# Kernel optimization log

Hardware: AMD Instinct MI355X
Metric: run time of the kernel (lower is better)

## Reference

```python
import jax, jax.numpy as jnp
import numpy as np

T, B, V, S = 800, 32, 1024, 100
BLANK = 0
LS = 0.1
NEG = -1e10  # finite 'log-zero' to keep grads NaN-free


def setup_inputs() -> dict:
    key = jax.random.key(0)
    k1, k2, k3, k4 = jax.random.split(key, 4)
    logits = jax.random.normal(k1, (T, B, V), jnp.float32)
    log_probs = jax.nn.log_softmax(logits, axis=-1)  # (T,B,V) as F.ctc_loss expects
    targets = jax.random.randint(k2, (B, S), 1, V)   # non-blank labels
    input_lengths = jax.random.randint(k3, (B,), T // 2, T + 1)
    target_lengths = jax.random.randint(k4, (B,), S // 2, S + 1)
    return dict(log_probs=log_probs, targets=targets,
                input_lengths=input_lengths, target_lengths=target_lengths)


def _ctc_loss_mean(log_probs, targets, input_lengths, target_lengths):
    # log_probs: (T,B,V); targets: (B,S)
    Tt, Bb, Vv = log_probs.shape
    Ss = targets.shape[1]
    L = 2 * Ss + 1  # extended label sequence: blank-interleaved
    ext = jnp.full((Bb, L), BLANK, dtype=targets.dtype).at[:, 1::2].set(targets)
    ext_prev2 = jnp.pad(ext[:, :-2], ((0, 0), (2, 0)), constant_values=BLANK)
    # transition s-2 -> s allowed only for non-blank labels differing from two back
    can_skip = (ext != BLANK) & (ext != ext_prev2)  # (B,L)

    def emit(lp_t):  # (B,V) -> (B,L) emission log-probs of extended labels
        return jnp.take_along_axis(lp_t, ext, axis=1)

    e0 = emit(log_probs[0])
    alpha0 = jnp.full((Bb, L), NEG, dtype=log_probs.dtype)
    alpha0 = alpha0.at[:, 0].set(e0[:, 0]).at[:, 1].set(e0[:, 1])

    def step(alpha, xs):
        lp_t, t = xs
        a1 = jnp.pad(alpha[:, :-1], ((0, 0), (1, 0)), constant_values=NEG)
        a2 = jnp.pad(alpha[:, :-2], ((0, 0), (2, 0)), constant_values=NEG)
        new = jnp.logaddexp(alpha, a1)
        new = jnp.where(can_skip, jnp.logaddexp(new, a2), new) + emit(lp_t)
        # freeze alpha for t >= input_length so final carry == alpha at len-1
        alpha = jnp.where((t < input_lengths)[:, None], new, alpha)
        return alpha, None

    alpha_T, _ = jax.lax.scan(step, alpha0, (log_probs[1:], jnp.arange(1, Tt)))

    idx = 2 * target_lengths  # final blank position in extended sequence
    a_blank = jnp.take_along_axis(alpha_T, idx[:, None], axis=1)[:, 0]
    a_label = jnp.take_along_axis(alpha_T, (idx - 1)[:, None], axis=1)[:, 0]
    nll = -jnp.logaddexp(a_blank, a_label)  # (B,)
    nll = jnp.where(nll > 1e9, 0.0, nll)    # zero_infinity
    # reduction='mean': per-sample loss / target_length, then batch mean
    return jnp.mean(nll / target_lengths.astype(log_probs.dtype))


def reference(log_probs, targets, input_lengths, target_lengths):
    ctc = _ctc_loss_mean(log_probs, targets, input_lengths, target_lengths)
    smooth = -jnp.mean(log_probs)
    return (1.0 - LS) * ctc + LS * smooth
```

## Files before the change

kernel.cpp:

```cpp
#include <hip/hip_runtime.h>
#include <hip/hip_bf16.h>

#define T_DIM 800
#define B_DIM 32
#define V_DIM 1024
#define S_DIM 100
#define L2E  1.4426950408889634f
#define LN2  0.6931471805599453f

#define NB1  1600
#define EOFF 4096
#define EROW 128
#define BROWS 801


__device__ __forceinline__ float dpp_shr1_f(float x) {
    return __int_as_float(__builtin_amdgcn_update_dpp(
        0, __float_as_int(x), 0x138, 0xF, 0xF, false));
}
__device__ __forceinline__ int dpp_shr1_i(int x) {
    return __builtin_amdgcn_update_dpp(0, x, 0x138, 0xF, 0xF, false);
}
__device__ __forceinline__ float rl50(float x) {
    return __int_as_float(__builtin_amdgcn_readlane(__float_as_int(x), 50));
}
__device__ __forceinline__ void gl16(const float* g, float* lds_dst) {
    __builtin_amdgcn_global_load_lds(
        (const __attribute__((address_space(1))) unsigned int*)g,
        (__attribute__((address_space(3))) unsigned int*)lds_dst,
        16, 0, 0);
}

extern "C" __global__ void __launch_bounds__(256)
ctc_prep(const float* __restrict__ lp,
         const int* __restrict__ tgt,
         float* __restrict__ ws)
{
    __shared__ float rb[4][V_DIM];
    __shared__ float red[4];
    float* E = ws + EOFF;
    float* partials = ws + 1;
    const int bid = blockIdx.x;
    const int tid = threadIdx.x;
    const int w = tid >> 6, j = tid & 63;
    const int b  = bid / 50;
    const int t0 = (bid - b * 50) * 16 + w * 4;
    const int* tg = tgt + b * S_DIM;

    if (bid == 0 && tid == 0) ((unsigned int*)ws)[0] = 0;

    int c1 = 0, c2 = 0;
    if (j <= 49) { int2 t2 = ((const int2*)tg)[j]; c1 = t2.x; c2 = t2.y; }

    const float* base = lp + ((size_t)t0 * B_DIM + b) * V_DIM;
    const size_t RSTRIDE = (size_t)B_DIM * V_DIM;

    const float4* s0 = (const float4*)base;
    float4 A = s0[j], Bv = s0[j + 64], C = s0[j + 128], D = s0[j + 192];

    float s = 0.0f;
    #pragma unroll
    for (int i = 0; i < 4; ++i) {
        float4 A2 = A, B2 = Bv, C2 = C, D2 = D;
        if (i < 3) {
            const float4* sn = (const float4*)(base + (size_t)(i + 1) * RSTRIDE);
            A2 = sn[j]; B2 = sn[j + 64]; C2 = sn[j + 128]; D2 = sn[j + 192];
        }
        s += ((A.x + A.y) + (A.z + A.w)) + ((Bv.x + Bv.y) + (Bv.z + Bv.w))
           + ((C.x + C.y) + (C.z + C.w)) + ((D.x + D.y) + (D.z + D.w));
        float* rw = rb[w];
        ((float4*)rw)[j] = A; ((float4*)rw)[j + 64] = Bv;
        ((float4*)rw)[j + 128] = C; ((float4*)rw)[j + 192] = D;
        float a, c;
        if (j <= 49)      { a = __builtin_amdgcn_exp2f(rw[c1] * L2E);
                            c = __builtin_amdgcn_exp2f(rw[c2] * L2E); }
        else if (j == 50) { float ebv = __builtin_amdgcn_exp2f(rw[0] * L2E);
                            a = ebv; c = ebv; }
        else              { a = 0.0f; c = 0.0f; }
        ((float2*)(E + ((size_t)b * BROWS + t0 + i) * EROW))[j] = make_float2(a, c);
        A = A2; Bv = B2; C = C2; D = D2;
    }
    for (int off = 32; off; off >>= 1) s += __shfl_down(s, off, 64);
    if (j == 0) red[w] = s;
    __syncthreads();
    if (tid == 0) partials[bid] = (red[0] + red[1]) + (red[2] + red[3]);
}

extern "C" __global__ void __launch_bounds__(128)
ctc_rec(const int* __restrict__ tgt,
        const int* __restrict__ ilen,
        const int* __restrict__ tlen,
        float* __restrict__ ws,
        float* __restrict__ out)
{
    __shared__ float bufA[32 * EROW];
    __shared__ float bufB[32 * EROW];
    unsigned int* cnt = (unsigned int*)ws;
    float* partials = ws + 1;
    float* nlls = ws + 1 + NB1;
    const int b = blockIdx.x;
    const int tid = threadIdx.x;
    const int wav = tid >> 6;
    const int l = tid & 63;
    const float* E = ws + EOFF + (size_t)b * BROWS * EROW;
    const int* tg = tgt + b * S_DIM;
    const int len = ilen[b];
    const int tl  = tlen[b];
    const int steps = len - 1;
    const int nfull = steps >> 5;
    const int nst   = steps & 31;
    const int N     = nfull + (nst ? 1 : 0);

#define STAGE_P(BUFP, SB) do { \
    const int tb_ = 1 + 32 * (SB); \
    float* bp_ = (BUFP); \
    _Pragma("unroll") \
    for (int g_ = 0; g_ < 16; ++g_) { \
        gl16(E + (size_t)(tb_ + 2 * g_) * EROW + 4 * l, bp_ + g_ * 256); \
    } \
} while (0)

#define WAIT0 do { \
    asm volatile("s_waitcnt vmcnt(0)" ::: "memory"); \
    __builtin_amdgcn_sched_barrier(0); \
} while (0)

    if (wav == 1) {
        STAGE_P(bufA, 0); WAIT0;
        __builtin_amdgcn_s_barrier();
        #pragma unroll 1
        for (int k = 1; k < N; ++k) {
            STAGE_P((k & 1) ? bufB : bufA, k); WAIT0;
            __builtin_amdgcn_s_barrier();
        }
        return;
    }

    float cs1f = 0, cs3f = 0;
    if (l <= 49) {
        int v1 = tg[2 * l];
        int vp = (l >= 1) ? tg[2 * l - 1] : -1;
        cs1f = (v1 != vp) ? 1.0f : 0.0f;
        int v3 = tg[2 * l + 1];
        cs3f = (v3 != v1) ? 1.0f : 0.0f;
    }

    float p0 = 0, p1 = 0, p2 = 0, p3 = 0;
    float qv = 0, sff = 0, sfg = 0;
    int   el = 0, eLp = 0;
    {
        float2 q0 = ((const float2*)E)[l];
        float eb0 = rl50(q0.x);
        p0 = (l == 0) ? eb0  : 0.0f;
        p1 = (l == 0) ? q0.x : 0.0f;
    }

    float2 ga0, ga1, ga2, ga3, gb0, gb1, gb2, gb3;

#define PREF_(BUF, G, R0, R1, R2, R3) do { \
    const float2* bp_ = (const float2*)(BUF); \
    R0 = bp_[(4 * (G) + 0) * 64 + l]; \
    R1 = bp_[(4 * (G) + 1) * 64 + l]; \
    R2 = bp_[(4 * (G) + 2) * 64 + l]; \
    R3 = bp_[(4 * (G) + 3) * 64 + l]; \
} while (0)

#define BD do { \
    float mz_ = fmaxf(fmaxf(p0, p1), fmaxf(p2, p3)); \
    int dead_ = (mz_ == 0.0f) ? 1 : 0; \
    int er_ = (int)((__float_as_uint(mz_) >> 23) & 255u); \
    unsigned fld_ = dead_ ? 127u : (unsigned)(254 - er_); \
    float sc_ = __uint_as_float(fld_ << 23); \
    p0 *= sc_; p1 *= sc_; p2 *= sc_; p3 *= sc_; \
    el += dead_ ? 0 : (er_ - 127); \
    int e1s_ = dpp_shr1_i(el); \
    int elA_ = dead_ ? e1s_ : el; \
    int e2s_ = dpp_shr1_i(elA_); \
    int elB_ = dead_ ? e2s_ : el; \
    int e3s_ = dpp_shr1_i(elB_); \
    int d1_ = e3s_ - elB_; d1_ = d1_ < -120 ? -120 : (d1_ > 120 ? 120 : d1_); \
    int d2_ = eLp  - elB_; d2_ = d2_ < -120 ? -120 : (d2_ > 120 ? 120 : d2_); \
    sfg = (l == 0) ? 0.0f : __uint_as_float((unsigned)(d1_ + 127) << 23); \
    sff = (l == 0) ? 0.0f : __uint_as_float((unsigned)(d2_ + 127) << 23); \
    el = elB_; eLp = e3s_; \
} while (0)

#define ST(SF, Q, EBS) do { \
    float h3_ = qv * (SF); \
    float vown_ = fmaf(cs3f, p1, p2 + p3); \
    float n3_ = vown_ * (Q).y; \
    float n0_ = (p0 + h3_) * (EBS); \
    float n1_ = fmaf(cs1f, h3_, p0 + p1) * (Q).x; \
    float n2_ = (p1 + p2) * (EBS); \
    qv = dpp_shr1_f(n3_); \
    p0 = n0_; p1 = n1_; p2 = n2_; p3 = n3_; \
} while (0)

#define GRP_(R0, R1, R2, R3) do { \
    BD; \
    ST(sff, R0, rl50(R0.x)); \
    ST(sfg, R1, rl50(R1.x)); \
    ST(sfg, R2, rl50(R2.x)); \
    ST(sfg, R3, rl50(R3.x)); \
} while (0)

#define GRPT_(R0, R1, R2, R3, BASE) do { \
    if ((BASE) < nst) { \
        BD; \
        ST(sff, R0, rl50(R0.x)); \
        if ((BASE) + 1 < nst) ST(sfg, R1, rl50(R1.x)); \
        if ((BASE) + 2 < nst) ST(sfg, R2, rl50(R2.x)); \
        if ((BASE) + 3 < nst) ST(sfg, R3, rl50(R3.x)); \
    } \
} while (0)

#define CONS_FULL(BUF) do { \
    PREF_(BUF, 0, ga0, ga1, ga2, ga3); \
    PREF_(BUF, 1, gb0, gb1, gb2, gb3); GRP_(ga0, ga1, ga2, ga3); \
    PREF_(BUF, 2, ga0, ga1, ga2, ga3); GRP_(gb0, gb1, gb2, gb3); \
    PREF_(BUF, 3, gb0, gb1, gb2, gb3); GRP_(ga0, ga1, ga2, ga3); \
    PREF_(BUF, 4, ga0, ga1, ga2, ga3); GRP_(gb0, gb1, gb2, gb3); \
    PREF_(BUF, 5, gb0, gb1, gb2, gb3); GRP_(ga0, ga1, ga2, ga3); \
    PREF_(BUF, 6, ga0, ga1, ga2, ga3); GRP_(gb0, gb1, gb2, gb3); \
    PREF_(BUF, 7, gb0, gb1, gb2, gb3); GRP_(ga0, ga1, ga2, ga3); \
    GRP_(gb0, gb1, gb2, gb3); \
} while (0)

#define CONS_TAIL(BUF) do { \
    PREF_(BUF, 0, ga0, ga1, ga2, ga3); \
    PREF_(BUF, 1, gb0, gb1, gb2, gb3); GRPT_(ga0, ga1, ga2, ga3, 0); \
    PREF_(BUF, 2, ga0, ga1, ga2, ga3); GRPT_(gb0, gb1, gb2, gb3, 4); \
    PREF_(BUF, 3, gb0, gb1, gb2, gb3); GRPT_(ga0, ga1, ga2, ga3, 8); \
    PREF_(BUF, 4, ga0, ga1, ga2, ga3); GRPT_(gb0, gb1, gb2, gb3, 12); \
    PREF_(BUF, 5, gb0, gb1, gb2, gb3); GRPT_(ga0, ga1, ga2, ga3, 16); \
    PREF_(BUF, 6, ga0, ga1, ga2, ga3); GRPT_(gb0, gb1, gb2, gb3, 20); \
    PREF_(BUF, 7, gb0, gb1, gb2, gb3); GRPT_(ga0, ga1, ga2, ga3, 24); \
    GRPT_(gb0, gb1, gb2, gb3, 28); \
} while (0)

    __builtin_amdgcn_s_barrier();
    #pragma unroll 1
    for (int k = 0; k + 1 < N; ++k) {
        const float* cur = (k & 1) ? bufB : bufA;
        CONS_FULL(cur);
        __builtin_amdgcn_s_barrier();
    }
    {
        const float* cur = ((N - 1) & 1) ? bufB : bufA;
        if (nst) { CONS_TAIL(cur); } else { CONS_FULL(cur); }
    }

    int idx = 2 * tl;
    int lanehi = idx >> 2, rhi = idx & 3;
    int lanelo = (idx - 1) >> 2, rlo = (idx - 1) & 3;
    float q0 = __shfl(p0, lanehi, 64), q1 = __shfl(p1, lanehi, 64);
    float q2 = __shfl(p2, lanehi, 64), q3 = __shfl(p3, lanehi, 64);
    int   eh = __shfl(el, lanehi, 64);
    float ph = (rhi == 0) ? q0 : (rhi == 1) ? q1 : (rhi == 2) ? q2 : q3;
    float g0 = __shfl(p0, lanelo, 64), g1 = __shfl(p1, lanelo, 64);
    float g2 = __shfl(p2, lanelo, 64), g3 = __shfl(p3, lanelo, 64);
    int   eo = __shfl(el, lanelo, 64);
    float pl = (rlo == 0) ? g0 : (rlo == 1) ? g1 : (rlo == 2) ? g2 : g3;
    float vhi = (ph > 0.0f) ? __builtin_amdgcn_logf(ph) + (float)eh : -3.0e9f;
    float vlo = (pl > 0.0f) ? __builtin_amdgcn_logf(pl) + (float)eo : -3.0e9f;
    float m = fmaxf(vhi, vlo);
    float d = fminf(vhi, vlo) - m;
    float ll2 = m + __builtin_amdgcn_logf(1.0f + __builtin_amdgcn_exp2f(d));
    float nll = -ll2 * LN2;
    if (!(nll < 1e9f)) nll = 0.0f;

    int last = 0;
    if (l == 0) {
        nlls[b] = nll;
        __threadfence();
        unsigned old = __hip_atomic_fetch_add(cnt, 1u, __ATOMIC_ACQ_REL,
                                              __HIP_MEMORY_SCOPE_AGENT);
        last = (old == B_DIM - 1) ? 1 : 0;
    }
    last = __shfl(last, 0, 64);
    if (last) {
        float ps = 0.0f;
        for (int i = l; i < NB1; i += 64) ps += partials[i];
        for (int off = 32; off; off >>= 1) ps += __shfl_down(ps, off, 64);
        float cs = 0.0f;
        if (l < B_DIM) cs = nlls[l] / (float)tlen[l];
        for (int off = 32; off; off >>= 1) cs += __shfl_down(cs, off, 64);
        if (l == 0) {
            float smooth = -ps / (float)((long long)T_DIM * B_DIM * V_DIM);
            float ctc = cs / (float)B_DIM;
            out[0] = 0.9f * ctc + 0.1f * smooth;
        }
    }
}

extern "C" void kernel_launch(void* const* d_in, const int* in_sizes, int n_in,
                              void* d_out, int out_size, void* d_ws, size_t ws_size,
                              hipStream_t stream) {
    const float* lp  = (const float*)d_in[0];
    const int* tgt   = (const int*)d_in[1];
    const int* ilen  = (const int*)d_in[2];
    const int* tlen  = (const int*)d_in[3];
    float* out = (float*)d_out;
    float* ws  = (float*)d_ws;
    ctc_prep<<<NB1, 256, 0, stream>>>(lp, tgt, ws);
    ctc_rec<<<B_DIM, 128, 0, stream>>>(tgt, ilen, tlen, ws, out);
}
```

Before: 63.67 us.

## Stage blank emissions in a separate LDS array and load whole chunk upfront

The prep kernel now also writes each blank emission into a compact per-batch array. The producer wave copies it into LDS alongside the main chunk, so the consumer reads the blank values as broadcast float4s instead of calling readlane on lane 50 every step. The consumer also loads all 32 time-steps of a chunk into registers at once rather than double-buffering two groups. The aim is to take readlane latency off the serial recurrence chain and hide LDS load latency, at the cost of many more live registers and extra code paths for buffer selection.

```diff
diff --git a/kernel.cpp b/kernel.cpp
--- a/kernel.cpp
+++ b/kernel.cpp
@@ -12,6 +12,8 @@
 #define EOFF 4096
 #define EROW 128
 #define BROWS 801
+#define EBOFF (EOFF + 32 * BROWS * EROW)
+#define EBSTR 896
 
 
 __device__ __forceinline__ float dpp_shr1_f(float x) {
@@ -29,6 +31,12 @@
         (const __attribute__((address_space(1))) unsigned int*)g,
         (__attribute__((address_space(3))) unsigned int*)lds_dst,
         16, 0, 0);
+}
+__device__ __forceinline__ void gl4(const float* g, float* lds_dst) {
+    __builtin_amdgcn_global_load_lds(
+        (const __attribute__((address_space(1))) unsigned int*)g,
+        (__attribute__((address_space(3))) unsigned int*)lds_dst,
+        4, 0, 0);
 }
 
 extern "C" __global__ void __launch_bounds__(256)
@@ -39,6 +47,7 @@
     __shared__ float rb[4][V_DIM];
     __shared__ float red[4];
     float* E = ws + EOFF;
+    float* EBp = ws + EBOFF;
     float* partials = ws + 1;
     const int bid = blockIdx.x;
     const int tid = threadIdx.x;
@@ -75,7 +84,8 @@
         if (j <= 49)      { a = __builtin_amdgcn_exp2f(rw[c1] * L2E);
                             c = __builtin_amdgcn_exp2f(rw[c2] * L2E); }
         else if (j == 50) { float ebv = __builtin_amdgcn_exp2f(rw[0] * L2E);
-                            a = ebv; c = ebv; }
+                            a = ebv; c = ebv;
+                            EBp[(size_t)b * EBSTR + t0 + i] = ebv; }
         else              { a = 0.0f; c = 0.0f; }
         ((float2*)(E + ((size_t)b * BROWS + t0 + i) * EROW))[j] = make_float2(a, c);
         A = A2; Bv = B2; C = C2; D = D2;
@@ -95,6 +105,8 @@
 {
     __shared__ float bufA[32 * EROW];
     __shared__ float bufB[32 * EROW];
+    __shared__ __align__(16) float ebA[64];
+    __shared__ __align__(16) float ebB[64];
     unsigned int* cnt = (unsigned int*)ws;
     float* partials = ws + 1;
     float* nlls = ws + 1 + NB1;
@@ -103,6 +115,7 @@
     const int wav = tid >> 6;
     const int l = tid & 63;
     const float* E = ws + EOFF + (size_t)b * BROWS * EROW;
+    const float* EBb = ws + EBOFF + (size_t)b * EBSTR;
     const int* tg = tgt + b * S_DIM;
     const int len = ilen[b];
     const int tl  = tlen[b];
@@ -111,13 +124,14 @@
     const int nst   = steps & 31;
     const int N     = nfull + (nst ? 1 : 0);
 
-#define STAGE_P(BUFP, SB) do { \
+#define STAGE_P(BUFP, EBP, SB) do { \
     const int tb_ = 1 + 32 * (SB); \
     float* bp_ = (BUFP); \
     _Pragma("unroll") \
     for (int g_ = 0; g_ < 16; ++g_) { \
         gl16(E + (size_t)(tb_ + 2 * g_) * EROW + 4 * l, bp_ + g_ * 256); \
     } \
+    gl4(EBb + tb_ + l, (EBP)); \
 } while (0)
 
 #define WAIT0 do { \
@@ -126,11 +140,12 @@
 } while (0)
 
     if (wav == 1) {
-        STAGE_P(bufA, 0); WAIT0;
+        STAGE_P(bufA, ebA, 0); WAIT0;
         __builtin_amdgcn_s_barrier();
         #pragma unroll 1
         for (int k = 1; k < N; ++k) {
-            STAGE_P((k & 1) ? bufB : bufA, k); WAIT0;
+            if (k & 1) { STAGE_P(bufB, ebB, k); } else { STAGE_P(bufA, ebA, k); }
+            WAIT0;
             __builtin_amdgcn_s_barrier();
         }
         return;
@@ -155,14 +170,24 @@
         p1 = (l == 0) ? q0.x : 0.0f;
     }
 
-    float2 ga0, ga1, ga2, ga3, gb0, gb1, gb2, gb3;
-
-#define PREF_(BUF, G, R0, R1, R2, R3) do { \
+    float2 g0r0, g0r1, g0r2, g0r3, g1r0, g1r1, g1r2, g1r3;
+    float2 g2r0, g2r1, g2r2, g2r3, g3r0, g3r1, g3r2, g3r3;
+    float2 g4r0, g4r1, g4r2, g4r3, g5r0, g5r1, g5r2, g5r3;
+    float2 g6r0, g6r1, g6r2, g6r3, g7r0, g7r1, g7r2, g7r3;
+    float4 eb40, eb41, eb42, eb43, eb44, eb45, eb46, eb47;
+
+#define LOADG(BUF, EBB, G) do { \
     const float2* bp_ = (const float2*)(BUF); \
-    R0 = bp_[(4 * (G) + 0) * 64 + l]; \
-    R1 = bp_[(4 * (G) + 1) * 64 + l]; \
-    R2 = bp_[(4 * (G) + 2) * 64 + l]; \
-    R3 = bp_[(4 * (G) + 3) * 64 + l]; \
+    g##G##r0 = bp_[(4 * G + 0) * 64 + l]; \
+    g##G##r1 = bp_[(4 * G + 1) * 64 + l]; \
+    g##G##r2 = bp_[(4 * G + 2) * 64 + l]; \
+    g##G##r3 = bp_[(4 * G + 3) * 64 + l]; \
+    eb4##G = ((const float4*)(EBB))[G]; \
+} while (0)
+
+#define LOADALL(BUF, EBB) do { \
+    LOADG(BUF, EBB, 0); LOADG(BUF, EBB, 1); LOADG(BUF, EBB, 2); LOADG(BUF, EBB, 3); \
+    LOADG(BUF, EBB, 4); LOADG(BUF, EBB, 5); LOADG(BUF, EBB, 6); LOADG(BUF, EBB, 7); \
 } while (0)
 
 #define BD do { \
@@ -196,58 +221,49 @@
     p0 = n0_; p1 = n1_; p2 = n2_; p3 = n3_; \
 } while (0)
 
-#define GRP_(R0, R1, R2, R3) do { \
+#define GRPX(G) do { \
     BD; \
-    ST(sff, R0, rl50(R0.x)); \
-    ST(sfg, R1, rl50(R1.x)); \
-    ST(sfg, R2, rl50(R2.x)); \
-    ST(sfg, R3, rl50(R3.x)); \
-} while (0)
-
-#define GRPT_(R0, R1, R2, R3, BASE) do { \
+    ST(sff, g##G##r0, eb4##G.x); \
+    ST(sfg, g##G##r1, eb4##G.y); \
+    ST(sfg, g##G##r2, eb4##G.z); \
+    ST(sfg, g##G##r3, eb4##G.w); \
+} while (0)
+
+#define GRPTX(G, BASE) do { \
     if ((BASE) < nst) { \
         BD; \
-        ST(sff, R0, rl50(R0.x)); \
-        if ((BASE) + 1 < nst) ST(sfg, R1, rl50(R1.x)); \
-        if ((BASE) + 2 < nst) ST(sfg, R2, rl50(R2.x)); \
-        if ((BASE) + 3 < nst) ST(sfg, R3, rl50(R3.x)); \
+        ST(sff, g##G##r0, eb4##G.x); \
+        if ((BASE) + 1 < nst) ST(sfg, g##G##r1, eb4##G.y); \
+        if ((BASE) + 2 < nst) ST(sfg, g##G##r2, eb4##G.z); \
+        if ((BASE) + 3 < nst) ST(sfg, g##G##r3, eb4##G.w); \
     } \
 } while (0)
 
-#define CONS_FULL(BUF) do { \
-    PREF_(BUF, 0, ga0, ga1, ga2, ga3); \
-    PREF_(BUF, 1, gb0, gb1, gb2, gb3); GRP_(ga0, ga1, ga2, ga3); \
-    PREF_(BUF, 2, ga0, ga1, ga2, ga3); GRP_(gb0, gb1, gb2, gb3); \
-    PREF_(BUF, 3, gb0, gb1, gb2, gb3); GRP_(ga0, ga1, ga2, ga3); \
-    PREF_(BUF, 4, ga0, ga1, ga2, ga3); GRP_(gb0, gb1, gb2, gb3); \
-    PREF_(BUF, 5, gb0, gb1, gb2, gb3); GRP_(ga0, ga1, ga2, ga3); \
-    PREF_(BUF, 6, ga0, ga1, ga2, ga3); GRP_(gb0, gb1, gb2, gb3); \
-    PREF_(BUF, 7, gb0, gb1, gb2, gb3); GRP_(ga0, ga1, ga2, ga3); \
-    GRP_(gb0, gb1, gb2, gb3); \
-} while (0)
-
-#define CONS_TAIL(BUF) do { \
-    PREF_(BUF, 0, ga0, ga1, ga2, ga3); \
-    PREF_(BUF, 1, gb0, gb1, gb2, gb3); GRPT_(ga0, ga1, ga2, ga3, 0); \
-    PREF_(BUF, 2, ga0, ga1, ga2, ga3); GRPT_(gb0, gb1, gb2, gb3, 4); \
-    PREF_(BUF, 3, gb0, gb1, gb2, gb3); GRPT_(ga0, ga1, ga2, ga3, 8); \
-    PREF_(BUF, 4, ga0, ga1, ga2, ga3); GRPT_(gb0, gb1, gb2, gb3, 12); \
-    PREF_(BUF, 5, gb0, gb1, gb2, gb3); GRPT_(ga0, ga1, ga2, ga3, 16); \
-    PREF_(BUF, 6, ga0, ga1, ga2, ga3); GRPT_(gb0, gb1, gb2, gb3, 20); \
-    PREF_(BUF, 7, gb0, gb1, gb2, gb3); GRPT_(ga0, ga1, ga2, ga3, 24); \
-    GRPT_(gb0, gb1, gb2, gb3, 28); \
+#define CONS_FULL(BUF, EBB) do { \
+    LOADALL(BUF, EBB); \
+    GRPX(0); GRPX(1); GRPX(2); GRPX(3); \
+    GRPX(4); GRPX(5); GRPX(6); GRPX(7); \
+} while (0)
+
+#define CONS_TAIL(BUF, EBB) do { \
+    LOADALL(BUF, EBB); \
+    GRPTX(0, 0);  GRPTX(1, 4);  GRPTX(2, 8);  GRPTX(3, 12); \
+    GRPTX(4, 16); GRPTX(5, 20); GRPTX(6, 24); GRPTX(7, 28); \
 } while (0)
 
     __builtin_amdgcn_s_barrier();
     #pragma unroll 1
     for (int k = 0; k + 1 < N; ++k) {
-        const float* cur = (k & 1) ? bufB : bufA;
-        CONS_FULL(cur);
+        if (k & 1) { CONS_FULL(bufB, ebB); } else { CONS_FULL(bufA, ebA); }
         __builtin_amdgcn_s_barrier();
     }
     {
-        const float* cur = ((N - 1) & 1) ? bufB : bufA;
-        if (nst) { CONS_TAIL(cur); } else { CONS_FULL(cur); }
+        const int kk = (N - 1) & 1;
+        if (nst) {
+            if (kk) { CONS_TAIL(bufB, ebB); } else { CONS_TAIL(bufA, ebA); }
+        } else {
+            if (kk) { CONS_FULL(bufB, ebB); } else { CONS_FULL(bufA, ebA); }
+        }
     }
 
     int idx = 2 * tl;
```

New measurement: 66.95 us. 5.1% more time.
